# Optimization experiments

Hardware: AMD Instinct MI355X
Metric: run time of the kernel (lower is better)

The kernel has to match this reference:

```python
import jax, jax.numpy as jnp
import numpy as np

NUM_V, NUM_R, ARITY = 100000, 1000, 3
D, I, H = 128, 64, 128
B, N = 4096, 64


def setup_inputs() -> dict:
    key = jax.random.key(0)
    ks = jax.random.split(key, 11)
    return {
        "r": jax.random.randint(ks[0], (B, N), 0, NUM_R),
        "e": jax.random.randint(ks[1], (ARITY, B, N), 0, NUM_V),
        "V": jax.random.normal(ks[2], (NUM_V, D + I), dtype=jnp.float32),
        "R": jax.random.normal(ks[3], (NUM_R, D), dtype=jnp.float32),
        "P": jax.random.normal(ks[4], (ARITY, D), dtype=jnp.float32),
        "WV": jax.random.normal(ks[5], (D + I, H), dtype=jnp.float32) * (1.0 / np.sqrt(D + I)),
        "bV": jax.random.normal(ks[6], (H,), dtype=jnp.float32) * 0.01,
        "WR": jax.random.normal(ks[7], (D, H), dtype=jnp.float32) * (1.0 / np.sqrt(D)),
        "bR": jax.random.normal(ks[8], (H,), dtype=jnp.float32) * 0.01,
        "WP": jax.random.normal(ks[9], (D, H), dtype=jnp.float32) * (1.0 / np.sqrt(D)),
        "bP": jax.random.normal(ks[10], (H,), dtype=jnp.float32) * 0.01,
    }


def reference(r, e, V, R, P, WV, bV, WR, bR, WP, bP):
    # x = Rl(R[r]) : gather relation embeddings then project -> [B, N, H]
    x = jnp.einsum("bnd,dh->bnh", R[r], WR) + bR
    # Pl(P[i]) for all arity positions at once -> [A, H]
    pe = P @ WP + bP
    # Vl(V[e[i]]) for all positions: gather then project -> [A, B, N, H]
    ve = jnp.einsum("abnd,dh->abnh", V[e], WV) + bV
    # loop body x = x * Pl(P[i]) * Vl(V[e[i]]) == product over arity axis
    x = x * jnp.prod(pe[:, None, None, :] * ve, axis=0)
    # dropout is identity (p=0 / eval); reduce over neighbor axis
    return jnp.sum(x, axis=1)  # [B, H]
```

## Files before the change

kernel.cpp:

```cpp
#include <hip/hip_runtime.h>

#define NUM_V 100000
#define NUM_R 1000
#define ARITY 3
#define DD 128
#define DI 192
#define HH 128
#define BB 4096
#define NN 64

typedef __attribute__((ext_vector_type(4))) float f32x4;
typedef __attribute__((ext_vector_type(8))) _Float16 half8;
typedef __attribute__((ext_vector_type(2))) _Float16 half2v;

__global__ __launch_bounds__(512, 4) void gemm_fused(
    const float* __restrict__ A, const float* __restrict__ WV, const float* __restrict__ bV,
    const float* __restrict__ R, const float* __restrict__ WR, const float* __restrict__ bR,
    const float* __restrict__ P, const float* __restrict__ WP, const float* __restrict__ bP,
    _Float16* __restrict__ VWh, _Float16* __restrict__ RWh, float* __restrict__ peProd,
    int M) {
    __shared__ unsigned short bsm[24576];

    const int tid = threadIdx.x;
    const int l = tid & 63;
    const int wv = tid >> 6;
    const int bid = blockIdx.x;

    const int tile = bid * 8 + wv;
    const int rowbase = tile * 16;
    const bool active = rowbase < M;

    const float* aptr;
    {
        int rr = rowbase + (l & 15);
        if (rr >= M) rr = M - 1;
        aptr = A + (size_t)rr * DI + (l >> 4) * 8;
    }

    f32x4 va[6][2];
#pragma unroll
    for (int ks = 0; ks < 6; ++ks) {
        va[ks][0] = *(const f32x4*)(aptr + ks * 32);
        va[ks][1] = *(const f32x4*)(aptr + ks * 32 + 4);
    }
    __builtin_amdgcn_sched_barrier(0);

    float bcol[8];
#pragma unroll
    for (int ct = 0; ct < 8; ++ct) bcol[ct] = bV[ct * 16 + (l & 15)];

#pragma unroll
    for (int i = 0; i < 6; ++i) {
        const int g = i * 512 + tid;
        const int ks = g >> 9;
        const int ct = (g >> 6) & 7;
        const int ln = g & 63;
        const int col = ct * 16 + (ln & 15);
        const int kbase = ks * 32 + ((ln >> 4) << 3);
        half8 hv;
#pragma unroll
        for (int j = 0; j < 8; ++j)
            hv[j] = (_Float16)WV[(size_t)(kbase + j) * HH + col];
        *(half8*)&bsm[(size_t)g * 8] = hv;
    }

    __syncthreads();

    if (active) {
        f32x4 acc[8];
#pragma unroll
        for (int ct = 0; ct < 8; ++ct) acc[ct] = (f32x4){0.f, 0.f, 0.f, 0.f};

#pragma unroll
        for (int ks = 0; ks < 6; ++ks) {
            half8 ah;
            {
                half8 t;
                t[0] = (_Float16)va[ks][0].x;
                t[1] = (_Float16)va[ks][0].y;
                t[2] = (_Float16)va[ks][0].z;
                t[3] = (_Float16)va[ks][0].w;
                t[4] = (_Float16)va[ks][1].x;
                t[5] = (_Float16)va[ks][1].y;
                t[6] = (_Float16)va[ks][1].z;
                t[7] = (_Float16)va[ks][1].w;
                ah = t;
            }
#pragma unroll
            for (int ct = 0; ct < 8; ++ct) {
                const int fb = (ks * 8 + ct) * 512;
                half8 bh = *(const half8*)&bsm[fb + l * 8];
                acc[ct] = __builtin_amdgcn_mfma_f32_16x16x32_f16(ah, bh, acc[ct], 0, 0, 0);
            }
        }

        const int rb = rowbase + (l >> 4) * 4;
#pragma unroll
        for (int j = 0; j < 4; ++j) {
            const int row = rb + j;
            if (row < M) {
#pragma unroll
                for (int ct = 0; ct < 8; ++ct)
                    VWh[(size_t)row * HH + ct * 16 + (l & 15)] = (_Float16)(acc[ct][j] + bcol[ct]);
            }
        }
    }

    if (bid < 500) {
        if (tid < 256) {
            const int row = bid * 2 + (tid >> 7);
            const int col = tid & 127;
            float a2 = bR[col];
            const float* Rr = R + (size_t)row * DD;
            for (int d = 0; d < DD; ++d) a2 += Rr[d] * WR[(size_t)d * HH + col];
            RWh[(size_t)row * HH + col] = (_Float16)a2;
        }
    } else if (bid == 501) {
        if (tid < HH) {
            const int h = tid;
            float prod = 1.0f;
            for (int a = 0; a < ARITY; ++a) {
                float a2 = bP[h];
                for (int d = 0; d < DD; ++d) a2 += P[a * DD + d] * WP[d * HH + h];
                prod *= a2;
            }
            peProd[h] = prod;
        }
    }
}

__global__ __launch_bounds__(256) void gather_kernel(const int* __restrict__ r,
                                                     const int* __restrict__ e,
                                                     const _Float16* __restrict__ VWh,
                                                     const _Float16* __restrict__ RWh,
                                                     const float* __restrict__ peProd,
                                                     float* __restrict__ out) {
    __shared__ int rIdx[NN];
    __shared__ int eIdx[ARITY][NN];
    __shared__ float4 partial[3][16][2];

    const int b = blockIdx.x;
    const int tid = threadIdx.x;

    if (tid < NN) {
        rIdx[tid] = r[b * NN + tid];
    } else {
        int t = tid - NN;
        eIdx[t >> 6][t & 63] = e[(size_t)(t >> 6) * BB * NN + b * NN + (t & 63)];
    }
    __syncthreads();

    const int lane = tid & 63;
    const int wv = tid >> 6;
    const int q = lane >> 4;
    const int ho = lane & 15;

    float acc8[8];
#pragma unroll
    for (int k = 0; k < 8; ++k) acc8[k] = 0.f;

#pragma unroll
    for (int it = 0; it < 4; ++it) {
        int n = it * 16 + wv * 4 + q;
        half8 rw = *(const half8*)(RWh + (size_t)rIdx[n] * HH + ho * 8);
        half8 v0 = *(const half8*)(VWh + (size_t)eIdx[0][n] * HH + ho * 8);
        half8 v1 = *(const half8*)(VWh + (size_t)eIdx[1][n] * HH + ho * 8);
        half8 v2 = *(const half8*)(VWh + (size_t)eIdx[2][n] * HH + ho * 8);
        half8 p = rw * v0;
        p = p * v1;
        p = p * v2;
#pragma unroll
        for (int k = 0; k < 8; ++k) acc8[k] += (float)p[k];
    }

#pragma unroll
    for (int k = 0; k < 8; ++k) {
        acc8[k] += __shfl_xor(acc8[k], 16);
        acc8[k] += __shfl_xor(acc8[k], 32);
    }

    if (wv > 0 && lane < 16) {
        partial[wv - 1][ho][0] = make_float4(acc8[0], acc8[1], acc8[2], acc8[3]);
        partial[wv - 1][ho][1] = make_float4(acc8[4], acc8[5], acc8[6], acc8[7]);
    }
    __syncthreads();
    if (wv == 0 && lane < 16) {
        float4 s0 = make_float4(acc8[0], acc8[1], acc8[2], acc8[3]);
        float4 s1 = make_float4(acc8[4], acc8[5], acc8[6], acc8[7]);
#pragma unroll
        for (int g = 0; g < 3; ++g) {
            float4 t0 = partial[g][ho][0], t1 = partial[g][ho][1];
            s0.x += t0.x; s0.y += t0.y; s0.z += t0.z; s0.w += t0.w;
            s1.x += t1.x; s1.y += t1.y; s1.z += t1.z; s1.w += t1.w;
        }
        float4 p0 = ((const float4*)peProd)[ho * 2];
        float4 p1 = ((const float4*)peProd)[ho * 2 + 1];
        ((float4*)(out + (size_t)b * HH))[ho * 2] =
            make_float4(s0.x * p0.x, s0.y * p0.y, s0.z * p0.z, s0.w * p0.w);
        ((float4*)(out + (size_t)b * HH))[ho * 2 + 1] =
            make_float4(s1.x * p1.x, s1.y * p1.y, s1.z * p1.z, s1.w * p1.w);
    }
}

extern "C" void kernel_launch(void* const* d_in, const int* in_sizes, int n_in,
                              void* d_out, int out_size, void* d_ws, size_t ws_size,
                              hipStream_t stream) {
    const int* r = (const int*)d_in[0];
    const int* e = (const int*)d_in[1];
    const float* V = (const float*)d_in[2];
    const float* R = (const float*)d_in[3];
    const float* P = (const float*)d_in[4];
    const float* WV = (const float*)d_in[5];
    const float* bV = (const float*)d_in[6];
    const float* WR = (const float*)d_in[7];
    const float* bR = (const float*)d_in[8];
    const float* WP = (const float*)d_in[9];
    const float* bP = (const float*)d_in[10];
    float* out = (float*)d_out;

    _Float16* VWh = (_Float16*)d_ws;
    _Float16* RWh = VWh + (size_t)NUM_V * HH;
    float* peProd = (float*)(RWh + (size_t)NUM_R * HH);

    const int tiles = (NUM_V + 15) / 16;
    gemm_fused<<<(tiles + 7) / 8, 512, 0, stream>>>(V, WV, bV, R, WR, bR, P, WP, bP,
                                                    VWh, RWh, peProd, NUM_V);
    gather_kernel<<<BB, 256, 0, stream>>>(r, e, VWh, RWh, peProd, out);
}
```

Baseline: 57.48 us.

## Make projection GEMM persistent with register double-buffered row tile prefetch

```diff
diff --git a/kernel.cpp b/kernel.cpp
--- a/kernel.cpp
+++ b/kernel.cpp
@@ -13,7 +13,7 @@
 typedef __attribute__((ext_vector_type(8))) _Float16 half8;
 typedef __attribute__((ext_vector_type(2))) _Float16 half2v;
 
-__global__ __launch_bounds__(512, 4) void gemm_fused(
+__global__ __launch_bounds__(512, 2) void gemm_fused(
     const float* __restrict__ A, const float* __restrict__ WV, const float* __restrict__ bV,
     const float* __restrict__ R, const float* __restrict__ WR, const float* __restrict__ bR,
     const float* __restrict__ P, const float* __restrict__ WP, const float* __restrict__ bP,
@@ -26,28 +26,56 @@
     const int wv = tid >> 6;
     const int bid = blockIdx.x;
 
-    const int tile = bid * 8 + wv;
-    const int rowbase = tile * 16;
-    const bool active = rowbase < M;
-
-    const float* aptr;
-    {
-        int rr = rowbase + (l & 15);
-        if (rr >= M) rr = M - 1;
-        aptr = A + (size_t)rr * DI + (l >> 4) * 8;
-    }
-
-    f32x4 va[6][2];
-#pragma unroll
-    for (int ks = 0; ks < 6; ++ks) {
-        va[ks][0] = *(const f32x4*)(aptr + ks * 32);
-        va[ks][1] = *(const f32x4*)(aptr + ks * 32 + 4);
-    }
+    const int slot = bid * 8 + wv;
+
+    float bcol[8];
+#pragma unroll
+    for (int ct = 0; ct < 8; ++ct) bcol[ct] = bV[ct * 16 + (l & 15)];
+
+    const float* abase = A + (size_t)(l & 15) * DI + (l >> 4) * 8;
+
+    f32x4 va[2][6][2];
+
+#define BURST(buf, t)                                                  \
+    do {                                                               \
+        const float* bp_ = abase + (size_t)(t) * (16 * DI);            \
+        _Pragma("unroll") for (int ks = 0; ks < 6; ++ks) {             \
+            va[buf][ks][0] = *(const f32x4*)(bp_ + ks * 32);           \
+            va[buf][ks][1] = *(const f32x4*)(bp_ + ks * 32 + 4);       \
+        }                                                              \
+    } while (0)
+
+#define COMPUTE(buf)                                                   \
+    _Pragma("unroll") for (int ks = 0; ks < 6; ++ks) {                 \
+        half8 ah;                                                      \
+        ah[0] = (_Float16)va[buf][ks][0].x;                            \
+        ah[1] = (_Float16)va[buf][ks][0].y;                            \
+        ah[2] = (_Float16)va[buf][ks][0].z;                            \
+        ah[3] = (_Float16)va[buf][ks][0].w;                            \
+        ah[4] = (_Float16)va[buf][ks][1].x;                            \
+        ah[5] = (_Float16)va[buf][ks][1].y;                            \
+        ah[6] = (_Float16)va[buf][ks][1].z;                            \
+        ah[7] = (_Float16)va[buf][ks][1].w;                            \
+        _Pragma("unroll") for (int ct = 0; ct < 8; ++ct) {             \
+            const int fb = (ks * 8 + ct) * 512;                        \
+            half8 bh = *(const half8*)&bsm[fb + l * 8];                \
+            acc[ct] = __builtin_amdgcn_mfma_f32_16x16x32_f16(ah, bh, acc[ct], 0, 0, 0); \
+        }                                                              \
+    }
+
+#define STORE(t)                                                       \
+    do {                                                               \
+        const int rb_ = (t) * 16 + ((l >> 4) << 2);                    \
+        _Pragma("unroll") for (int j = 0; j < 4; ++j) {                \
+            _Pragma("unroll") for (int ct = 0; ct < 8; ++ct)           \
+                VWh[(size_t)(rb_ + j) * HH + ct * 16 + (l & 15)] =     \
+                    (_Float16)(acc[ct][j] + bcol[ct]);                 \
+        }                                                              \
+    } while (0)
+
+    BURST(0, slot);
+    BURST(1, slot + 2048);
     __builtin_amdgcn_sched_barrier(0);
-
-    float bcol[8];
-#pragma unroll
-    for (int ct = 0; ct < 8; ++ct) bcol[ct] = bV[ct * 16 + (l & 15)];
 
 #pragma unroll
     for (int i = 0; i < 6; ++i) {
@@ -66,56 +94,56 @@
 
     __syncthreads();
 
-    if (active) {
-        f32x4 acc[8];
-#pragma unroll
-        for (int ct = 0; ct < 8; ++ct) acc[ct] = (f32x4){0.f, 0.f, 0.f, 0.f};
-
-#pragma unroll
-        for (int ks = 0; ks < 6; ++ks) {
-            half8 ah;
-            {
-                half8 t;
-                t[0] = (_Float16)va[ks][0].x;
-                t[1] = (_Float16)va[ks][0].y;
-                t[2] = (_Float16)va[ks][0].z;
-                t[3] = (_Float16)va[ks][0].w;
-                t[4] = (_Float16)va[ks][1].x;
-                t[5] = (_Float16)va[ks][1].y;
-                t[6] = (_Float16)va[ks][1].z;
-                t[7] = (_Float16)va[ks][1].w;
-                ah = t;
-            }
-#pragma unroll
-            for (int ct = 0; ct < 8; ++ct) {
-                const int fb = (ks * 8 + ct) * 512;
-                half8 bh = *(const half8*)&bsm[fb + l * 8];
-                acc[ct] = __builtin_amdgcn_mfma_f32_16x16x32_f16(ah, bh, acc[ct], 0, 0, 0);
-            }
+    {
+        f32x4 acc[8];
+#pragma unroll
+        for (int ct = 0; ct < 8; ++ct) acc[ct] = (f32x4){0.f, 0.f, 0.f, 0.f};
+        COMPUTE(0);
+        BURST(0, slot + 4096);
+        __builtin_amdgcn_sched_barrier(0);
+        STORE(slot);
+    }
+
+    {
+        f32x4 acc[8];
+#pragma unroll
+        for (int ct = 0; ct < 8; ++ct) acc[ct] = (f32x4){0.f, 0.f, 0.f, 0.f};
+        COMPUTE(1);
+        if (slot < 106) {
+            BURST(1, slot + 6144);
         }
-
-        const int rb = rowbase + (l >> 4) * 4;
-#pragma unroll
-        for (int j = 0; j < 4; ++j) {
-            const int row = rb + j;
-            if (row < M) {
-#pragma unroll
-                for (int ct = 0; ct < 8; ++ct)
-                    VWh[(size_t)row * HH + ct * 16 + (l & 15)] = (_Float16)(acc[ct][j] + bcol[ct]);
-            }
-        }
-    }
-
-    if (bid < 500) {
-        if (tid < 256) {
-            const int row = bid * 2 + (tid >> 7);
-            const int col = tid & 127;
-            float a2 = bR[col];
-            const float* Rr = R + (size_t)row * DD;
-            for (int d = 0; d < DD; ++d) a2 += Rr[d] * WR[(size_t)d * HH + col];
-            RWh[(size_t)row * HH + col] = (_Float16)a2;
-        }
-    } else if (bid == 501) {
+        __builtin_amdgcn_sched_barrier(0);
+        STORE(slot + 2048);
+    }
+
+    {
+        f32x4 acc[8];
+#pragma unroll
+        for (int ct = 0; ct < 8; ++ct) acc[ct] = (f32x4){0.f, 0.f, 0.f, 0.f};
+        COMPUTE(0);
+        STORE(slot + 4096);
+    }
+
+    if (slot < 106) {
+        f32x4 acc[8];
+#pragma unroll
+        for (int ct = 0; ct < 8; ++ct) acc[ct] = (f32x4){0.f, 0.f, 0.f, 0.f};
+        COMPUTE(1);
+        STORE(slot + 6144);
+    }
+
+#undef BURST
+#undef COMPUTE
+#undef STORE
+
+    if (bid < 250) {
+        const int row = bid * 4 + (tid >> 7);
+        const int col = tid & 127;
+        float a2 = bR[col];
+        const float* Rr = R + (size_t)row * DD;
+        for (int d = 0; d < DD; ++d) a2 += Rr[d] * WR[(size_t)d * HH + col];
+        RWh[(size_t)row * HH + col] = (_Float16)a2;
+    } else if (bid == 255) {
         if (tid < HH) {
             const int h = tid;
             float prod = 1.0f;
@@ -222,8 +250,7 @@
     _Float16* RWh = VWh + (size_t)NUM_V * HH;
     float* peProd = (float*)(RWh + (size_t)NUM_R * HH);
 
-    const int tiles = (NUM_V + 15) / 16;
-    gemm_fused<<<(tiles + 7) / 8, 512, 0, stream>>>(V, WV, bV, R, WR, bR, P, WP, bP,
-                                                    VWh, RWh, peProd, NUM_V);
+    gemm_fused<<<256, 512, 0, stream>>>(V, WV, bV, R, WR, bR, P, WP, bP,
+                                        VWh, RWh, peProd, NUM_V);
     gather_kernel<<<BB, 256, 0, stream>>>(r, e, VWh, RWh, peProd, out);
 }
```

Measured after the change: 58.02 us. No clear change (+0.9%).
